# Performance work log

Hardware: AMD Instinct MI355X
Metric: run time of the kernel (lower is better)

Reference implementation:

```python
import jax, jax.numpy as jnp
from jax import lax
import numpy as np

T_IN, T_OUT, B, N, H, DIN, DOUT = 32, 32, 64, 64, 128, 1, 1


def _w(k, shape):
    s = 1.0 / np.sqrt(shape[0])
    return jax.random.uniform(k, shape, jnp.float32, -s, s)


def setup_inputs() -> dict:
    key = jax.random.key(0)
    ks = jax.random.split(key, 16)
    inputs_enc = jax.random.normal(ks[0], (T_IN, B, N, DIN), jnp.float32)
    targets = jax.random.normal(ks[1], (T_OUT, B, N, DOUT), jnp.float32)
    A = jax.random.uniform(ks[2], (B, N, N), jnp.float32)
    supports = A / jnp.sum(A, axis=-1, keepdims=True)  # row-normalized adjacency
    out = {"inputs_enc": inputs_enc, "targets": targets, "supports": supports}
    # GCGRU cells: encoder layer0 (Din=DIN), encoder layer1 (Din=H),
    # decoder layer0 (Din=DOUT), decoder shared base cell (Din=H)
    i = 3
    for name, din in (("e0", DIN), ("e1", H), ("d0", DOUT), ("db", H)):
        out[name + "_Wru"] = _w(ks[i], (din + H, 2 * H)); i += 1
        out[name + "_bru"] = jnp.zeros((2 * H,), jnp.float32)
        out[name + "_Wc"] = _w(ks[i], (din + H, H)); i += 1
        out[name + "_bc"] = jnp.zeros((H,), jnp.float32)
    out["Wp"] = _w(ks[i], (H, DOUT))
    out["bp"] = jnp.zeros((DOUT,), jnp.float32)
    return out


def gcgru(supports, x, h, Wru, bru, Wc, bc):
    # supports: [B,N,N], x: [B,N,Din], h: [B,N,H]
    cat = jnp.concatenate([x, h], axis=-1)
    g = jax.nn.sigmoid(jnp.einsum('bij,bjd->bid', supports, cat) @ Wru + bru)
    r, u = jnp.split(g, 2, axis=-1)
    cat2 = jnp.concatenate([x, r * h], axis=-1)
    c = jnp.tanh(jnp.einsum('bij,bjd->bid', supports, cat2) @ Wc + bc)
    return u * h + (1.0 - u) * c


def reference(inputs_enc, targets, supports,
              e0_Wru, e0_bru, e0_Wc, e0_bc,
              e1_Wru, e1_bru, e1_Wc, e1_bc,
              d0_Wru, d0_bru, d0_Wc, d0_bc,
              db_Wru, db_bru, db_Wc, db_bc,
              Wp, bp):
    b, n = supports.shape[0], supports.shape[1]
    h = e0_Wc.shape[1]
    dout = Wp.shape[1]
    t_out = targets.shape[0]
    dt = inputs_enc.dtype

    def enc_layer(xs, p):
        def step(hs, x):
            hn = gcgru(supports, x, hs, *p)
            return hn, hn
        return lax.scan(step, jnp.zeros((b, n, h), dt), xs)

    hT0, hs0 = enc_layer(inputs_enc, (e0_Wru, e0_bru, e0_Wc, e0_bc))
    hT1, _ = enc_layer(hs0, (e1_Wru, e1_bru, e1_Wc, e1_bc))

    go = jnp.zeros((b, n, dout), dt)

    def dec_step(carry, _):
        h0, h1, cur = carry
        hn0 = gcgru(supports, cur, h0, d0_Wru, d0_bru, d0_Wc, d0_bc)
        hn1 = gcgru(supports, hn0, h1, db_Wru, db_bru, db_Wc, db_bc)
        proj = hn1 @ Wp + bp  # [B,N,DOUT]
        return (hn0, hn1, proj), proj.reshape(b, n * dout)

    _, outs = lax.scan(dec_step, (hT0, hT1, go), None, length=t_out)
    return outs  # [T_out, B, N*DOUT]
```

## Files before the change

### kernel.cpp

```cpp
#include <hip/hip_runtime.h>


#define LDS_FLOATS 33344
#define LDS_BYTES  (LDS_FLOATS * 4)

#define H0p (L + 0)
#define H1p (L + 8192)
#define B1p (L + 16384)
#define B2p (L + 24576)
#define XSp (L + 32768)
#define MPp (L + 32832)

struct KParams {
  const float* inp;
  const float* S;
  const float* w[16];
  const float* Wp;
  const float* bp;
  float* out;
  float* stg;
};

__device__ __forceinline__ float sigm(float v) { return 1.f / (1.f + __expf(-v)); }

__device__ __forceinline__ void mixt(float* __restrict__ dst, const float* __restrict__ src,
                                     const float* __restrict__ stb, int tid)
{
  const int n0 = (tid & 15) * 4, f0 = (tid >> 4) * 4;
  float acc[4][4];
  #pragma unroll
  for (int i = 0; i < 4; ++i)
    #pragma unroll
    for (int j = 0; j < 4; ++j) acc[i][j] = 0.f;
  #pragma unroll 4
  for (int m = 0; m < 64; ++m) {
    const float4 a4 = *(const float4*)&src[m * 128 + f0];
    const float4 b4 = *(const float4*)&stb[m * 64 + n0];
    const float av[4] = {a4.x, a4.y, a4.z, a4.w};
    const float bv[4] = {b4.x, b4.y, b4.z, b4.w};
    #pragma unroll
    for (int i = 0; i < 4; ++i)
      #pragma unroll
      for (int j = 0; j < 4; ++j) acc[i][j] += av[i] * bv[j];
  }
  #pragma unroll
  for (int i = 0; i < 4; ++i)
    *(float4*)&dst[(f0 + i) * 64 + n0] = make_float4(acc[i][0], acc[i][1], acc[i][2], acc[i][3]);
}

__device__ __forceinline__ void accum_ru(const float* __restrict__ Mt, const float* __restrict__ w1,
    float racc[4][4], float uacc[4][4], int r0, int c)
{
  #pragma unroll 4
  for (int kk = 0; kk < 128; ++kk) {
    const float4 a4 = *(const float4*)&Mt[kk * 64 + r0];
    const float4 wr = *(const float4*)&w1[kk * 256 + c];
    const float4 wu = *(const float4*)&w1[kk * 256 + 128 + c];
    const float av[4] = {a4.x, a4.y, a4.z, a4.w};
    const float wrv[4] = {wr.x, wr.y, wr.z, wr.w};
    const float wuv[4] = {wu.x, wu.y, wu.z, wu.w};
    #pragma unroll
    for (int i = 0; i < 4; ++i)
      #pragma unroll
      for (int j = 0; j < 4; ++j) {
        racc[i][j] += av[i] * wrv[j];
        uacc[i][j] += av[i] * wuv[j];
      }
  }
}

__device__ __forceinline__ void accum_ruc(const float* __restrict__ Mt, const float* __restrict__ w1,
    const float* __restrict__ w2, float racc[4][4], float uacc[4][4], float cacc[4][4], int r0, int c)
{
  #pragma unroll 4
  for (int kk = 0; kk < 128; ++kk) {
    const float4 a4 = *(const float4*)&Mt[kk * 64 + r0];
    const float4 wr = *(const float4*)&w1[kk * 256 + c];
    const float4 wu = *(const float4*)&w1[kk * 256 + 128 + c];
    const float4 wc = *(const float4*)&w2[kk * 128 + c];
    const float av[4] = {a4.x, a4.y, a4.z, a4.w};
    const float wrv[4] = {wr.x, wr.y, wr.z, wr.w};
    const float wuv[4] = {wu.x, wu.y, wu.z, wu.w};
    const float wcv[4] = {wc.x, wc.y, wc.z, wc.w};
    #pragma unroll
    for (int i = 0; i < 4; ++i)
      #pragma unroll
      for (int j = 0; j < 4; ++j) {
        racc[i][j] += av[i] * wrv[j];
        uacc[i][j] += av[i] * wuv[j];
        cacc[i][j] += av[i] * wcv[j];
      }
  }
}

__device__ __forceinline__ void accum_c(const float* __restrict__ Mt, const float* __restrict__ w2,
    float cacc[4][4], int r0, int c)
{
  #pragma unroll 4
  for (int kk = 0; kk < 128; ++kk) {
    const float4 a4 = *(const float4*)&Mt[kk * 64 + r0];
    const float4 wc = *(const float4*)&w2[kk * 128 + c];
    const float av[4] = {a4.x, a4.y, a4.z, a4.w};
    const float wcv[4] = {wc.x, wc.y, wc.z, wc.w};
    #pragma unroll
    for (int i = 0; i < 4; ++i)
      #pragma unroll
      for (int j = 0; j < 4; ++j) cacc[i][j] += av[i] * wcv[j];
  }
}

__device__ __forceinline__ void cell_tail(float* __restrict__ L, float* __restrict__ h,
    const float* __restrict__ stb, const float* __restrict__ wc_h,
    const float* __restrict__ bru, const float* __restrict__ bc,
    float racc[4][4], float uacc[4][4], float cacc[4][4], int tid)
{
  const int c = (tid & 31) * 4, r0 = (tid >> 5) * 4;
  const float4 bq1 = *(const float4*)&bru[c];
  const float4 bq2 = *(const float4*)&bru[128 + c];
  const float b1v[4] = {bq1.x, bq1.y, bq1.z, bq1.w};
  const float b2v[4] = {bq2.x, bq2.y, bq2.z, bq2.w};
  float r_[4][4], u_[4][4];
  #pragma unroll
  for (int i = 0; i < 4; ++i)
    #pragma unroll
    for (int j = 0; j < 4; ++j) {
      r_[i][j] = sigm(racc[i][j] + b1v[j]);
      u_[i][j] = sigm(uacc[i][j] + b2v[j]);
    }
  __syncthreads();
  #pragma unroll
  for (int i = 0; i < 4; ++i) {
    const float4 h4 = *(const float4*)&h[(r0 + i) * 128 + c];
    *(float4*)&B2p[(r0 + i) * 128 + c] =
        make_float4(r_[i][0] * h4.x, r_[i][1] * h4.y, r_[i][2] * h4.z, r_[i][3] * h4.w);
  }
  __syncthreads();
  mixt(B1p, B2p, stb, tid);
  __syncthreads();
  accum_c(B1p, wc_h, cacc, r0, c);
  const float4 bq3 = *(const float4*)&bc[c];
  const float b3v[4] = {bq3.x, bq3.y, bq3.z, bq3.w};
  #pragma unroll
  for (int i = 0; i < 4; ++i) {
    const float4 h4 = *(const float4*)&h[(r0 + i) * 128 + c];
    const float hv[4] = {h4.x, h4.y, h4.z, h4.w};
    float nv[4];
    #pragma unroll
    for (int j = 0; j < 4; ++j) {
      float cv = tanhf(cacc[i][j] + b3v[j]);
      nv[j] = u_[i][j] * hv[j] + (1.f - u_[i][j]) * cv;
    }
    *(float4*)&h[(r0 + i) * 128 + c] = make_float4(nv[0], nv[1], nv[2], nv[3]);
  }
  __syncthreads();
}

__device__ __forceinline__ void cell_dense(float* __restrict__ L, int tid,
    const float* __restrict__ x, float* __restrict__ h,
    const float* __restrict__ Wru, const float* __restrict__ bru,
    const float* __restrict__ Wc, const float* __restrict__ bc,
    const float* __restrict__ stb)
{
  mixt(B2p, x, stb, tid);
  mixt(B1p, h, stb, tid);
  __syncthreads();
  const int c = (tid & 31) * 4, r0 = (tid >> 5) * 4;
  float racc[4][4] = {{0.f}}, uacc[4][4] = {{0.f}}, cacc[4][4] = {{0.f}};
  accum_ruc(B2p, Wru, Wc, racc, uacc, cacc, r0, c);
  accum_ru(B1p, Wru + 128 * 256, racc, uacc, r0, c);
  cell_tail(L, h, stb, Wc + 128 * 128, bru, bc, racc, uacc, cacc, tid);
}

__device__ __forceinline__ void cell_sparse(float* __restrict__ L, int tid,
    const float* __restrict__ xg, bool hasx, float* __restrict__ h,
    const float* __restrict__ Wru, const float* __restrict__ bru,
    const float* __restrict__ Wc, const float* __restrict__ bc,
    const float* __restrict__ stb, const float* __restrict__ Sb)
{
  if (xg && tid < 64) XSp[tid] = xg[tid];
  mixt(B1p, h, stb, tid);
  __syncthreads();
  const int c = (tid & 31) * 4, r0 = (tid >> 5) * 4;
  if (hasx) {
    const int q = tid & 7, rr = tid >> 3;
    const float* srow = Sb + rr * 64 + q * 8;
    const float* xv = XSp + q * 8;
    const float4 s0 = *(const float4*)&srow[0];
    const float4 s1 = *(const float4*)&srow[4];
    MPp[q * 64 + rr] = s0.x * xv[0] + s0.y * xv[1] + s0.z * xv[2] + s0.w * xv[3]
                     + s1.x * xv[4] + s1.y * xv[5] + s1.z * xv[6] + s1.w * xv[7];
  }
  float racc[4][4] = {{0.f}}, uacc[4][4] = {{0.f}}, cacc[4][4] = {{0.f}};
  accum_ru(B1p, Wru + 256, racc, uacc, r0, c);
  __syncthreads();
  if (hasx) {
    float4 mv = make_float4(0.f, 0.f, 0.f, 0.f);
    #pragma unroll
    for (int q = 0; q < 8; ++q) {
      const float4 m4 = *(const float4*)&MPp[q * 64 + r0];
      mv.x += m4.x; mv.y += m4.y; mv.z += m4.z; mv.w += m4.w;
    }
    const float mva[4] = {mv.x, mv.y, mv.z, mv.w};
    const float4 w0r = *(const float4*)&Wru[c];
    const float4 w0u = *(const float4*)&Wru[128 + c];
    const float4 w0c = *(const float4*)&Wc[c];
    const float w0rv[4] = {w0r.x, w0r.y, w0r.z, w0r.w};
    const float w0uv[4] = {w0u.x, w0u.y, w0u.z, w0u.w};
    const float w0cv[4] = {w0c.x, w0c.y, w0c.z, w0c.w};
    #pragma unroll
    for (int i = 0; i < 4; ++i)
      #pragma unroll
      for (int j = 0; j < 4; ++j) {
        racc[i][j] += mva[i] * w0rv[j];
        uacc[i][j] += mva[i] * w0uv[j];
        cacc[i][j] += mva[i] * w0cv[j];
      }
  }
  cell_tail(L, h, stb, Wc + 128, bru, bc, racc, uacc, cacc, tid);
}

__device__ __forceinline__ void proj(float* __restrict__ L, const float* __restrict__ Wp,
    const float* __restrict__ bp, float* __restrict__ outg, int tid)
{
  const int n = tid & 63, q = tid >> 6;
  const float* hp = H1p + n * 128 + q * 16;
  const float* wp = Wp + q * 16;
  float s = 0.f;
  #pragma unroll
  for (int m = 0; m < 16; m += 4) {
    const float4 h4 = *(const float4*)&hp[m];
    const float4 w4 = *(const float4*)&wp[m];
    s += h4.x * w4.x + h4.y * w4.y + h4.z * w4.z + h4.w * w4.w;
  }
  MPp[q * 64 + n] = s;
  __syncthreads();
  if (tid < 64) {
    float v = bp[0];
    #pragma unroll
    for (int q2 = 0; q2 < 8; ++q2) v += MPp[q2 * 64 + tid];
    outg[tid] = v;
    XSp[tid] = v;
  }
  __syncthreads();
}

__global__ __launch_bounds__(512, 2) void gcgru_persist(KParams p)
{
  extern __shared__ float L[];
  const int b = blockIdx.x, tid = threadIdx.x;
  for (int i = tid; i < 16384; i += 512) L[i] = 0.f;
  const float* Sb = p.S + (size_t)b * 4096;
  float* stb = p.stg + (size_t)b * 4096;
  for (int idx = tid; idx < 4096; idx += 512)
    stb[idx] = Sb[(idx & 63) * 64 + (idx >> 6)];
  __syncthreads();

  for (int t = 0; t < 32; ++t) {
    cell_sparse(L, tid, p.inp + ((size_t)t * 64 + b) * 64, true, H0p,
                p.w[0], p.w[1], p.w[2], p.w[3], stb, Sb);
    cell_dense(L, tid, H0p, H1p, p.w[4], p.w[5], p.w[6], p.w[7], stb);
  }
  for (int t = 0; t < 32; ++t) {
    cell_sparse(L, tid, nullptr, t > 0, H0p,
                p.w[8], p.w[9], p.w[10], p.w[11], stb, Sb);
    cell_dense(L, tid, H0p, H1p, p.w[12], p.w[13], p.w[14], p.w[15], stb);
    proj(L, p.Wp, p.bp, p.out + (size_t)t * 4096 + (size_t)b * 64, tid);
  }
}

extern "C" void kernel_launch(void* const* d_in, const int* in_sizes, int n_in,
                              void* d_out, int out_size, void* d_ws, size_t ws_size,
                              hipStream_t stream)
{
  KParams p;
  p.inp = (const float*)d_in[0];
  p.S   = (const float*)d_in[2];
  for (int i = 0; i < 16; ++i) p.w[i] = (const float*)d_in[3 + i];
  p.Wp = (const float*)d_in[19];
  p.bp = (const float*)d_in[20];
  p.out = (float*)d_out;
  p.stg = (float*)d_ws;

  (void)hipFuncSetAttribute((const void*)gcgru_persist,
                            hipFuncAttributeMaxDynamicSharedMemorySize, LDS_BYTES);
  gcgru_persist<<<dim3(64), dim3(512), LDS_BYTES, stream>>>(p);
}
```

Before: 8.265 ms.

## Restructure GCGRU persistent kernel with 1024 threads, swizzled LDS state, LDS-resident supports

Rewrites the persistent kernel to use 1024 threads per block. Each thread owns one node lane and an 8-feature slice, so weight reads are wavefront-uniform broadcasts and the support-matrix read is a scalar per lane. The hidden states are stored in LDS with an XOR swizzle to avoid bank conflicts, and the transposed support matrix now lives in LDS instead of global workspace. The dense cell no longer mixes x and h in parallel; it mixes them one after the other through a single buffer, which adds extra barriers. The wider block raises register pressure and may reduce per-thread reuse compared with the previous 4x4 register tiles.

```diff
diff --git a/kernel.cpp b/kernel.cpp
--- a/kernel.cpp
+++ b/kernel.cpp
@@ -1,15 +1,15 @@
 #include <hip/hip_runtime.h>
 
 
-#define LDS_FLOATS 33344
-#define LDS_BYTES  (LDS_FLOATS * 4)
-
-#define H0p (L + 0)
-#define H1p (L + 8192)
-#define B1p (L + 16384)
-#define B2p (L + 24576)
-#define XSp (L + 32768)
-#define MPp (L + 32832)
+#define O_H0   0
+#define O_H1   8192
+#define O_RH   16384
+#define O_MT   24576
+#define O_STB  32768
+#define O_XS   36864
+#define O_MP   36928
+#define LDS_FLOATS 37952
+#define LDS_BYTES (LDS_FLOATS * 4)
 
 struct KParams {
   const float* inp;
@@ -18,253 +18,205 @@
   const float* Wp;
   const float* bp;
   float* out;
-  float* stg;
 };
 
 __device__ __forceinline__ float sigm(float v) { return 1.f / (1.f + __expf(-v)); }
 
-__device__ __forceinline__ void mixt(float* __restrict__ dst, const float* __restrict__ src,
-                                     const float* __restrict__ stb, int tid)
-{
-  const int n0 = (tid & 15) * 4, f0 = (tid >> 4) * 4;
-  float acc[4][4];
+__device__ __forceinline__ int sidx(int n, int f0) {
+  return n * 128 + ((((f0 >> 2) ^ (n & 31)) & 31) << 2);
+}
+
+__device__ __forceinline__ void mixt(float* __restrict__ L, const float* __restrict__ src,
+                                     int lane, int f0)
+{
+  const float* stb = L + O_STB;
+  float acc[8] = {0.f, 0.f, 0.f, 0.f, 0.f, 0.f, 0.f, 0.f};
+  const int g0 = f0 >> 2;
+  #pragma unroll 4
+  for (int m = 0; m < 64; ++m) {
+    const float sv = stb[m * 64 + lane];
+    const float4 a = *(const float4*)&src[m * 128 + (((g0 ^ (m & 31)) & 31) << 2)];
+    const float4 b = *(const float4*)&src[m * 128 + ((((g0 + 1) ^ (m & 31)) & 31) << 2)];
+    acc[0] += a.x * sv; acc[1] += a.y * sv; acc[2] += a.z * sv; acc[3] += a.w * sv;
+    acc[4] += b.x * sv; acc[5] += b.y * sv; acc[6] += b.z * sv; acc[7] += b.w * sv;
+  }
+  float* MT = L + O_MT;
   #pragma unroll
-  for (int i = 0; i < 4; ++i)
+  for (int j = 0; j < 8; ++j) MT[(f0 + j) * 64 + lane] = acc[j];
+}
+
+#define FMA8(ACC, V0, V1) \
+  ACC[0] += p * V0.x; ACC[1] += p * V0.y; ACC[2] += p * V0.z; ACC[3] += p * V0.w; \
+  ACC[4] += p * V1.x; ACC[5] += p * V1.y; ACC[6] += p * V1.z; ACC[7] += p * V1.w;
+
+__device__ __forceinline__ void accum_ruc(const float* __restrict__ MT,
+    const float* __restrict__ wr, const float* __restrict__ wc,
+    float racc[8], float uacc[8], float cacc[8], int lane)
+{
+  #pragma unroll 4
+  for (int kk = 0; kk < 128; ++kk) {
+    const float p = MT[kk * 64 + lane];
+    const float4 r0 = *(const float4*)&wr[kk * 256];
+    const float4 r1 = *(const float4*)&wr[kk * 256 + 4];
+    const float4 u0 = *(const float4*)&wr[kk * 256 + 128];
+    const float4 u1 = *(const float4*)&wr[kk * 256 + 132];
+    const float4 c0 = *(const float4*)&wc[kk * 128];
+    const float4 c1 = *(const float4*)&wc[kk * 128 + 4];
+    FMA8(racc, r0, r1)
+    FMA8(uacc, u0, u1)
+    FMA8(cacc, c0, c1)
+  }
+}
+
+__device__ __forceinline__ void accum_ru(const float* __restrict__ MT,
+    const float* __restrict__ wr, float racc[8], float uacc[8], int lane)
+{
+  #pragma unroll 4
+  for (int kk = 0; kk < 128; ++kk) {
+    const float p = MT[kk * 64 + lane];
+    const float4 r0 = *(const float4*)&wr[kk * 256];
+    const float4 r1 = *(const float4*)&wr[kk * 256 + 4];
+    const float4 u0 = *(const float4*)&wr[kk * 256 + 128];
+    const float4 u1 = *(const float4*)&wr[kk * 256 + 132];
+    FMA8(racc, r0, r1)
+    FMA8(uacc, u0, u1)
+  }
+}
+
+__device__ __forceinline__ void accum_c(const float* __restrict__ MT,
+    const float* __restrict__ wc, float cacc[8], int lane)
+{
+  #pragma unroll 4
+  for (int kk = 0; kk < 128; ++kk) {
+    const float p = MT[kk * 64 + lane];
+    const float4 c0 = *(const float4*)&wc[kk * 128];
+    const float4 c1 = *(const float4*)&wc[kk * 128 + 4];
+    FMA8(cacc, c0, c1)
+  }
+}
+
+__device__ __forceinline__ void cell_tail(float* __restrict__ L, float* __restrict__ H,
+    const float* __restrict__ wc_h, const float* __restrict__ bru, const float* __restrict__ bc,
+    float racc[8], float uacc[8], float cacc[8], int lane, int f0)
+{
+  float rr[8], uu[8];
+  #pragma unroll
+  for (int j = 0; j < 8; ++j) {
+    rr[j] = sigm(racc[j] + bru[f0 + j]);
+    uu[j] = sigm(uacc[j] + bru[128 + f0 + j]);
+  }
+  float* RH = L + O_RH;
+  const int i0 = sidx(lane, f0), i1 = sidx(lane, f0 + 4);
+  float4 h0 = *(float4*)&H[i0], h1 = *(float4*)&H[i1];
+  *(float4*)&RH[i0] = make_float4(rr[0] * h0.x, rr[1] * h0.y, rr[2] * h0.z, rr[3] * h0.w);
+  *(float4*)&RH[i1] = make_float4(rr[4] * h1.x, rr[5] * h1.y, rr[6] * h1.z, rr[7] * h1.w);
+  __syncthreads();
+  mixt(L, L + O_RH, lane, f0);
+  __syncthreads();
+  accum_c(L + O_MT, wc_h, cacc, lane);
+  float cv[8];
+  #pragma unroll
+  for (int j = 0; j < 8; ++j) cv[j] = tanhf(cacc[j] + bc[f0 + j]);
+  h0.x = uu[0] * h0.x + (1.f - uu[0]) * cv[0];
+  h0.y = uu[1] * h0.y + (1.f - uu[1]) * cv[1];
+  h0.z = uu[2] * h0.z + (1.f - uu[2]) * cv[2];
+  h0.w = uu[3] * h0.w + (1.f - uu[3]) * cv[3];
+  h1.x = uu[4] * h1.x + (1.f - uu[4]) * cv[4];
+  h1.y = uu[5] * h1.y + (1.f - uu[5]) * cv[5];
+  h1.z = uu[6] * h1.z + (1.f - uu[6]) * cv[6];
+  h1.w = uu[7] * h1.w + (1.f - uu[7]) * cv[7];
+  *(float4*)&H[i0] = h0;
+  *(float4*)&H[i1] = h1;
+  __syncthreads();
+}
+
+__device__ __forceinline__ void cell_dense(float* __restrict__ L, int lane, int f0,
+    const float* __restrict__ Wru, const float* __restrict__ bru,
+    const float* __restrict__ Wc, const float* __restrict__ bc)
+{
+  mixt(L, L + O_H0, lane, f0);
+  __syncthreads();
+  float racc[8] = {0.f}, uacc[8] = {0.f}, cacc[8] = {0.f};
+  accum_ruc(L + O_MT, Wru + f0, Wc + f0, racc, uacc, cacc, lane);
+  __syncthreads();
+  mixt(L, L + O_H1, lane, f0);
+  __syncthreads();
+  accum_ru(L + O_MT, Wru + 128 * 256 + f0, racc, uacc, lane);
+  cell_tail(L, L + O_H1, Wc + 128 * 128 + f0, bru, bc, racc, uacc, cacc, lane, f0);
+}
+
+__device__ __forceinline__ void cell_sparse(float* __restrict__ L, int lane, int f0, bool hasx,
+    const float* __restrict__ Wru, const float* __restrict__ bru,
+    const float* __restrict__ Wc, const float* __restrict__ bc)
+{
+  mixt(L, L + O_H0, lane, f0);
+  __syncthreads();
+  float racc[8] = {0.f}, uacc[8] = {0.f}, cacc[8] = {0.f};
+  accum_ru(L + O_MT, Wru + 256 + f0, racc, uacc, lane);
+  if (hasx) {
+    const float* stb = L + O_STB;
+    const float* XS = L + O_XS;
+    float mxv = 0.f;
+    #pragma unroll 4
+    for (int m = 0; m < 64; m += 4) {
+      const float4 x4 = *(const float4*)&XS[m];
+      mxv += stb[(m + 0) * 64 + lane] * x4.x + stb[(m + 1) * 64 + lane] * x4.y
+           + stb[(m + 2) * 64 + lane] * x4.z + stb[(m + 3) * 64 + lane] * x4.w;
+    }
     #pragma unroll
-    for (int j = 0; j < 4; ++j) acc[i][j] = 0.f;
-  #pragma unroll 4
-  for (int m = 0; m < 64; ++m) {
-    const float4 a4 = *(const float4*)&src[m * 128 + f0];
-    const float4 b4 = *(const float4*)&stb[m * 64 + n0];
-    const float av[4] = {a4.x, a4.y, a4.z, a4.w};
-    const float bv[4] = {b4.x, b4.y, b4.z, b4.w};
-    #pragma unroll
-    for (int i = 0; i < 4; ++i)
-      #pragma unroll
-      for (int j = 0; j < 4; ++j) acc[i][j] += av[i] * bv[j];
-  }
-  #pragma unroll
-  for (int i = 0; i < 4; ++i)
-    *(float4*)&dst[(f0 + i) * 64 + n0] = make_float4(acc[i][0], acc[i][1], acc[i][2], acc[i][3]);
-}
-
-__device__ __forceinline__ void accum_ru(const float* __restrict__ Mt, const float* __restrict__ w1,
-    float racc[4][4], float uacc[4][4], int r0, int c)
-{
-  #pragma unroll 4
-  for (int kk = 0; kk < 128; ++kk) {
-    const float4 a4 = *(const float4*)&Mt[kk * 64 + r0];
-    const float4 wr = *(const float4*)&w1[kk * 256 + c];
-    const float4 wu = *(const float4*)&w1[kk * 256 + 128 + c];
-    const float av[4] = {a4.x, a4.y, a4.z, a4.w};
-    const float wrv[4] = {wr.x, wr.y, wr.z, wr.w};
-    const float wuv[4] = {wu.x, wu.y, wu.z, wu.w};
-    #pragma unroll
-    for (int i = 0; i < 4; ++i)
-      #pragma unroll
-      for (int j = 0; j < 4; ++j) {
-        racc[i][j] += av[i] * wrv[j];
-        uacc[i][j] += av[i] * wuv[j];
-      }
-  }
-}
-
-__device__ __forceinline__ void accum_ruc(const float* __restrict__ Mt, const float* __restrict__ w1,
-    const float* __restrict__ w2, float racc[4][4], float uacc[4][4], float cacc[4][4], int r0, int c)
-{
-  #pragma unroll 4
-  for (int kk = 0; kk < 128; ++kk) {
-    const float4 a4 = *(const float4*)&Mt[kk * 64 + r0];
-    const float4 wr = *(const float4*)&w1[kk * 256 + c];
-    const float4 wu = *(const float4*)&w1[kk * 256 + 128 + c];
-    const float4 wc = *(const float4*)&w2[kk * 128 + c];
-    const float av[4] = {a4.x, a4.y, a4.z, a4.w};
-    const float wrv[4] = {wr.x, wr.y, wr.z, wr.w};
-    const float wuv[4] = {wu.x, wu.y, wu.z, wu.w};
-    const float wcv[4] = {wc.x, wc.y, wc.z, wc.w};
-    #pragma unroll
-    for (int i = 0; i < 4; ++i)
-      #pragma unroll
-      for (int j = 0; j < 4; ++j) {
-        racc[i][j] += av[i] * wrv[j];
-        uacc[i][j] += av[i] * wuv[j];
-        cacc[i][j] += av[i] * wcv[j];
-      }
-  }
-}
-
-__device__ __forceinline__ void accum_c(const float* __restrict__ Mt, const float* __restrict__ w2,
-    float cacc[4][4], int r0, int c)
-{
-  #pragma unroll 4
-  for (int kk = 0; kk < 128; ++kk) {
-    const float4 a4 = *(const float4*)&Mt[kk * 64 + r0];
-    const float4 wc = *(const float4*)&w2[kk * 128 + c];
-    const float av[4] = {a4.x, a4.y, a4.z, a4.w};
-    const float wcv[4] = {wc.x, wc.y, wc.z, wc.w};
-    #pragma unroll
-    for (int i = 0; i < 4; ++i)
-      #pragma unroll
-      for (int j = 0; j < 4; ++j) cacc[i][j] += av[i] * wcv[j];
-  }
-}
-
-__device__ __forceinline__ void cell_tail(float* __restrict__ L, float* __restrict__ h,
-    const float* __restrict__ stb, const float* __restrict__ wc_h,
-    const float* __restrict__ bru, const float* __restrict__ bc,
-    float racc[4][4], float uacc[4][4], float cacc[4][4], int tid)
-{
-  const int c = (tid & 31) * 4, r0 = (tid >> 5) * 4;
-  const float4 bq1 = *(const float4*)&bru[c];
-  const float4 bq2 = *(const float4*)&bru[128 + c];
-  const float b1v[4] = {bq1.x, bq1.y, bq1.z, bq1.w};
-  const float b2v[4] = {bq2.x, bq2.y, bq2.z, bq2.w};
-  float r_[4][4], u_[4][4];
-  #pragma unroll
-  for (int i = 0; i < 4; ++i)
-    #pragma unroll
-    for (int j = 0; j < 4; ++j) {
-      r_[i][j] = sigm(racc[i][j] + b1v[j]);
-      u_[i][j] = sigm(uacc[i][j] + b2v[j]);
+    for (int j = 0; j < 8; ++j) {
+      racc[j] += mxv * Wru[f0 + j];
+      uacc[j] += mxv * Wru[128 + f0 + j];
+      cacc[j] += mxv * Wc[f0 + j];
     }
-  __syncthreads();
-  #pragma unroll
-  for (int i = 0; i < 4; ++i) {
-    const float4 h4 = *(const float4*)&h[(r0 + i) * 128 + c];
-    *(float4*)&B2p[(r0 + i) * 128 + c] =
-        make_float4(r_[i][0] * h4.x, r_[i][1] * h4.y, r_[i][2] * h4.z, r_[i][3] * h4.w);
-  }
-  __syncthreads();
-  mixt(B1p, B2p, stb, tid);
-  __syncthreads();
-  accum_c(B1p, wc_h, cacc, r0, c);
-  const float4 bq3 = *(const float4*)&bc[c];
-  const float b3v[4] = {bq3.x, bq3.y, bq3.z, bq3.w};
-  #pragma unroll
-  for (int i = 0; i < 4; ++i) {
-    const float4 h4 = *(const float4*)&h[(r0 + i) * 128 + c];
-    const float hv[4] = {h4.x, h4.y, h4.z, h4.w};
-    float nv[4];
-    #pragma unroll
-    for (int j = 0; j < 4; ++j) {
-      float cv = tanhf(cacc[i][j] + b3v[j]);
-      nv[j] = u_[i][j] * hv[j] + (1.f - u_[i][j]) * cv;
-    }
-    *(float4*)&h[(r0 + i) * 128 + c] = make_float4(nv[0], nv[1], nv[2], nv[3]);
-  }
-  __syncthreads();
-}
-
-__device__ __forceinline__ void cell_dense(float* __restrict__ L, int tid,
-    const float* __restrict__ x, float* __restrict__ h,
-    const float* __restrict__ Wru, const float* __restrict__ bru,
-    const float* __restrict__ Wc, const float* __restrict__ bc,
-    const float* __restrict__ stb)
-{
-  mixt(B2p, x, stb, tid);
-  mixt(B1p, h, stb, tid);
-  __syncthreads();
-  const int c = (tid & 31) * 4, r0 = (tid >> 5) * 4;
-  float racc[4][4] = {{0.f}}, uacc[4][4] = {{0.f}}, cacc[4][4] = {{0.f}};
-  accum_ruc(B2p, Wru, Wc, racc, uacc, cacc, r0, c);
-  accum_ru(B1p, Wru + 128 * 256, racc, uacc, r0, c);
-  cell_tail(L, h, stb, Wc + 128 * 128, bru, bc, racc, uacc, cacc, tid);
-}
-
-__device__ __forceinline__ void cell_sparse(float* __restrict__ L, int tid,
-    const float* __restrict__ xg, bool hasx, float* __restrict__ h,
-    const float* __restrict__ Wru, const float* __restrict__ bru,
-    const float* __restrict__ Wc, const float* __restrict__ bc,
-    const float* __restrict__ stb, const float* __restrict__ Sb)
-{
-  if (xg && tid < 64) XSp[tid] = xg[tid];
-  mixt(B1p, h, stb, tid);
-  __syncthreads();
-  const int c = (tid & 31) * 4, r0 = (tid >> 5) * 4;
-  if (hasx) {
-    const int q = tid & 7, rr = tid >> 3;
-    const float* srow = Sb + rr * 64 + q * 8;
-    const float* xv = XSp + q * 8;
-    const float4 s0 = *(const float4*)&srow[0];
-    const float4 s1 = *(const float4*)&srow[4];
-    MPp[q * 64 + rr] = s0.x * xv[0] + s0.y * xv[1] + s0.z * xv[2] + s0.w * xv[3]
-                     + s1.x * xv[4] + s1.y * xv[5] + s1.z * xv[6] + s1.w * xv[7];
-  }
-  float racc[4][4] = {{0.f}}, uacc[4][4] = {{0.f}}, cacc[4][4] = {{0.f}};
-  accum_ru(B1p, Wru + 256, racc, uacc, r0, c);
-  __syncthreads();
-  if (hasx) {
-    float4 mv = make_float4(0.f, 0.f, 0.f, 0.f);
-    #pragma unroll
-    for (int q = 0; q < 8; ++q) {
-      const float4 m4 = *(const float4*)&MPp[q * 64 + r0];
-      mv.x += m4.x; mv.y += m4.y; mv.z += m4.z; mv.w += m4.w;
-    }
-    const float mva[4] = {mv.x, mv.y, mv.z, mv.w};
-    const float4 w0r = *(const float4*)&Wru[c];
-    const float4 w0u = *(const float4*)&Wru[128 + c];
-    const float4 w0c = *(const float4*)&Wc[c];
-    const float w0rv[4] = {w0r.x, w0r.y, w0r.z, w0r.w};
-    const float w0uv[4] = {w0u.x, w0u.y, w0u.z, w0u.w};
-    const float w0cv[4] = {w0c.x, w0c.y, w0c.z, w0c.w};
-    #pragma unroll
-    for (int i = 0; i < 4; ++i)
-      #pragma unroll
-      for (int j = 0; j < 4; ++j) {
-        racc[i][j] += mva[i] * w0rv[j];
-        uacc[i][j] += mva[i] * w0uv[j];
-        cacc[i][j] += mva[i] * w0cv[j];
-      }
-  }
-  cell_tail(L, h, stb, Wc + 128, bru, bc, racc, uacc, cacc, tid);
-}
-
-__device__ __forceinline__ void proj(float* __restrict__ L, const float* __restrict__ Wp,
-    const float* __restrict__ bp, float* __restrict__ outg, int tid)
-{
-  const int n = tid & 63, q = tid >> 6;
-  const float* hp = H1p + n * 128 + q * 16;
-  const float* wp = Wp + q * 16;
-  float s = 0.f;
-  #pragma unroll
-  for (int m = 0; m < 16; m += 4) {
-    const float4 h4 = *(const float4*)&hp[m];
-    const float4 w4 = *(const float4*)&wp[m];
-    s += h4.x * w4.x + h4.y * w4.y + h4.z * w4.z + h4.w * w4.w;
-  }
-  MPp[q * 64 + n] = s;
-  __syncthreads();
-  if (tid < 64) {
+  }
+  cell_tail(L, L + O_H0, Wc + 128 + f0, bru, bc, racc, uacc, cacc, lane, f0);
+}
+
+__device__ __forceinline__ void proj(float* __restrict__ L, int lane, int f0,
+    const float* __restrict__ Wp, const float* __restrict__ bp, float* __restrict__ outg)
+{
+  const float* H = L + O_H1;
+  const int i0 = sidx(lane, f0), i1 = sidx(lane, f0 + 4);
+  const float4 h0 = *(const float4*)&H[i0], h1 = *(const float4*)&H[i1];
+  const float4 w0 = *(const float4*)&Wp[f0], w1 = *(const float4*)&Wp[f0 + 4];
+  (L + O_MP)[(f0 >> 3) * 64 + lane] =
+      h0.x * w0.x + h0.y * w0.y + h0.z * w0.z + h0.w * w0.w +
+      h1.x * w1.x + h1.y * w1.y + h1.z * w1.z + h1.w * w1.w;
+  __syncthreads();
+  if (threadIdx.x < 64) {
+    const float* MP = L + O_MP;
     float v = bp[0];
     #pragma unroll
-    for (int q2 = 0; q2 < 8; ++q2) v += MPp[q2 * 64 + tid];
-    outg[tid] = v;
-    XSp[tid] = v;
-  }
-  __syncthreads();
-}
-
-__global__ __launch_bounds__(512, 2) void gcgru_persist(KParams p)
+    for (int w2 = 0; w2 < 16; ++w2) v += MP[w2 * 64 + lane];
+    outg[lane] = v;
+    (L + O_XS)[lane] = v;
+  }
+  __syncthreads();
+}
+
+__global__ __launch_bounds__(1024, 4) void gcgru_persist(KParams p)
 {
   extern __shared__ float L[];
-  const int b = blockIdx.x, tid = threadIdx.x;
-  for (int i = tid; i < 16384; i += 512) L[i] = 0.f;
+  const int tid = threadIdx.x, b = blockIdx.x;
+  const int lane = tid & 63;
+  const int f0 = (tid >> 6) * 8;
+
+  for (int i = tid; i < 16384; i += 1024) L[i] = 0.f;
   const float* Sb = p.S + (size_t)b * 4096;
-  float* stb = p.stg + (size_t)b * 4096;
-  for (int idx = tid; idx < 4096; idx += 512)
-    stb[idx] = Sb[(idx & 63) * 64 + (idx >> 6)];
+  for (int i = tid; i < 4096; i += 1024)
+    (L + O_STB)[i] = Sb[(i & 63) * 64 + (i >> 6)];
   __syncthreads();
 
   for (int t = 0; t < 32; ++t) {
-    cell_sparse(L, tid, p.inp + ((size_t)t * 64 + b) * 64, true, H0p,
-                p.w[0], p.w[1], p.w[2], p.w[3], stb, Sb);
-    cell_dense(L, tid, H0p, H1p, p.w[4], p.w[5], p.w[6], p.w[7], stb);
+    if (tid < 64) (L + O_XS)[tid] = p.inp[((size_t)t * 64 + b) * 64 + tid];
+    cell_sparse(L, lane, f0, true, p.w[0], p.w[1], p.w[2], p.w[3]);
+    cell_dense (L, lane, f0,       p.w[4], p.w[5], p.w[6], p.w[7]);
   }
   for (int t = 0; t < 32; ++t) {
-    cell_sparse(L, tid, nullptr, t > 0, H0p,
-                p.w[8], p.w[9], p.w[10], p.w[11], stb, Sb);
-    cell_dense(L, tid, H0p, H1p, p.w[12], p.w[13], p.w[14], p.w[15], stb);
-    proj(L, p.Wp, p.bp, p.out + (size_t)t * 4096 + (size_t)b * 64, tid);
+    cell_sparse(L, lane, f0, t > 0, p.w[8],  p.w[9],  p.w[10], p.w[11]);
+    cell_dense (L, lane, f0,        p.w[12], p.w[13], p.w[14], p.w[15]);
+    proj(L, lane, f0, p.Wp, p.bp, p.out + (size_t)t * 4096 + (size_t)b * 64);
   }
 }
 
@@ -279,9 +231,8 @@
   p.Wp = (const float*)d_in[19];
   p.bp = (const float*)d_in[20];
   p.out = (float*)d_out;
-  p.stg = (float*)d_ws;
 
   (void)hipFuncSetAttribute((const void*)gcgru_persist,
                             hipFuncAttributeMaxDynamicSharedMemorySize, LDS_BYTES);
-  gcgru_persist<<<dim3(64), dim3(512), LDS_BYTES, stream>>>(p);
-}
+  gcgru_persist<<<dim3(64), dim3(1024), LDS_BYTES, stream>>>(p);
+}
```

After: 18.48 ms. +123.6%, slower.
